# Kernel tuning notes

Hardware: AMD Instinct MI355X
Metric: run time of the kernel (lower is better)

Reference implementation:

```python
import jax, jax.numpy as jnp
import numpy as np

D_MODEL, D_K, D_V, N_HEADS = 1024, 64, 64, 16
BATCH, N_CTX = 2, 2048


def half_causal_allowed(n):
    # rows [0, n/2): attend to cols [0, n/2) only (dense block)
    # rows [n/2, n): standard causal (col <= row)
    i = jnp.arange(n)[:, None]
    j = jnp.arange(n)[None, :]
    top = (i < n // 2) & (j < n // 2)
    bot = (i >= n // 2) & (j <= i)
    return top | bot  # [n, n] bool


def setup_inputs() -> dict:
    key = jax.random.key(0)
    ks = jax.random.split(key, 8)
    s_in = 1.0 / np.sqrt(D_MODEL)
    s_out = 1.0 / np.sqrt(D_V * N_HEADS)
    return {
        "x": jax.random.normal(ks[0], (BATCH, N_CTX, D_MODEL), jnp.float32),
        # Linear weights stored [in, out] (transpose of torch layout)
        "Wq": jax.random.uniform(ks[1], (D_MODEL, D_K * N_HEADS), jnp.float32, -s_in, s_in),
        "bq": jax.random.uniform(ks[2], (D_K * N_HEADS,), jnp.float32, -s_in, s_in),
        "Wk": jax.random.uniform(ks[3], (D_MODEL, D_K * N_HEADS), jnp.float32, -s_in, s_in),
        "bk": jax.random.uniform(ks[4], (D_K * N_HEADS,), jnp.float32, -s_in, s_in),
        "Wv": jax.random.uniform(ks[5], (D_MODEL, D_V * N_HEADS), jnp.float32, -s_in, s_in),
        "bv": jax.random.uniform(ks[6], (D_V * N_HEADS,), jnp.float32, -s_in, s_in),
        "Wo": jax.random.uniform(ks[7], (D_V * N_HEADS, D_MODEL), jnp.float32, -s_out, s_out),
    }


def reference(x, Wq, bq, Wk, bk, Wv, bv, Wo):
    b, n, _ = x.shape
    h, dk, dv = N_HEADS, D_K, D_V
    # projections -> [b, h, n, d]
    q = (x @ Wq + bq).reshape(b, n, h, dk).transpose(0, 2, 1, 3)
    k = (x @ Wk + bk).reshape(b, n, h, dk).transpose(0, 2, 1, 3)
    v = (x @ Wv + bv).reshape(b, n, h, dv).transpose(0, 2, 1, 3)
    scores = jnp.einsum("bhqd,bhkd->bhqk", q / jnp.sqrt(jnp.float32(dk)), k)
    allowed = half_causal_allowed(n)  # [n, n]
    scores = jnp.where(allowed, scores, -jnp.inf)
    attn = jax.nn.softmax(scores, axis=-1)  # dropout p=0 -> identity
    out = jnp.einsum("bhqk,bhkd->bhqd", attn, v)
    out = out.transpose(0, 2, 1, 3).reshape(b, n, h * dv)
    return out @ Wo  # final Linear has no bias
```

## Files before the change

kernel.cpp:

```cpp
#include <hip/hip_runtime.h>
#include <hip/hip_bf16.h>

#define NH 16
#define DH 64
#define DM 1024
#define NC 2048
#define MROWS 4096
#define KVT 64

#define SCALE_Q 0.180336880f

typedef __attribute__((ext_vector_type(8))) short short8;
typedef __attribute__((ext_vector_type(4))) float f32x4;
typedef __attribute__((ext_vector_type(16))) float f32x16;
typedef __attribute__((ext_vector_type(4))) unsigned int uint4e;

__device__ __forceinline__ unsigned pkbf16(float a, float b) {
    unsigned r;
    asm("v_cvt_pk_bf16_f32 %0, %1, %2" : "=v"(r) : "v"(a), "v"(b));
    return r;
}
__device__ __forceinline__ unsigned short f2bf(float x) {
    return (unsigned short)(pkbf16(x, x) & 0xffffu);
}
__device__ __forceinline__ float exp2v(float x) {
    float r;
    asm("v_exp_f32 %0, %1" : "=v"(r) : "v"(x));
    return r;
}
__device__ __forceinline__ f32x16 fzero16() {
    f32x16 r;
    #pragma unroll
    for (int i = 0; i < 16; ++i) r[i] = 0.f;
    return r;
}
__device__ __forceinline__ short8 mk8(unsigned w0, unsigned w1, unsigned w2, unsigned w3) {
    uint4e u = {w0, w1, w2, w3};
    return __builtin_bit_cast(short8, u);
}
__device__ __forceinline__ void gload16(const unsigned short* g, unsigned short* l) {
    __builtin_amdgcn_global_load_lds(
        (const __attribute__((address_space(1))) void*)g,
        (__attribute__((address_space(3))) void*)l, 16, 0, 0);
}

__global__ __launch_bounds__(256) void cvt_x(const float* __restrict__ in,
                                             unsigned short* __restrict__ out, int n8)
{
    int i = blockIdx.x * 256 + threadIdx.x;
    if (i >= n8) return;
    const float4 a = ((const float4*)in)[i * 2];
    const float4 b = ((const float4*)in)[i * 2 + 1];
    uint4e u = {pkbf16(a.x, a.y), pkbf16(a.z, a.w), pkbf16(b.x, b.y), pkbf16(b.z, b.w)};
    ((uint4e*)out)[i] = u;
}

__global__ __launch_bounds__(256) void cvt_w4(const float* __restrict__ W0,
                                              const float* __restrict__ W1,
                                              const float* __restrict__ W2,
                                              const float* __restrict__ W3,
                                              unsigned short* __restrict__ Wt4)
{
    __shared__ unsigned short T[64][72];
    const int z = blockIdx.z;
    const float* W = (z == 0) ? W0 : (z == 1) ? W1 : (z == 2) ? W2 : W3;
    unsigned short* Wt = Wt4 + (size_t)z * DM * DM;
    const int t = threadIdx.x;
    const int r = t >> 2, s = t & 3;
    const int bi = blockIdx.y;
    const int bj = blockIdx.x;
    const float* src = W + (size_t)(bi * 64 + r) * DM + bj * 64 + s * 16;
    float4 f0 = ((const float4*)src)[0];
    float4 f1 = ((const float4*)src)[1];
    float4 f2 = ((const float4*)src)[2];
    float4 f3 = ((const float4*)src)[3];
    uint2 u;
    u.x = pkbf16(f0.x, f0.y); u.y = pkbf16(f0.z, f0.w); *(uint2*)&T[r][s * 16]      = u;
    u.x = pkbf16(f1.x, f1.y); u.y = pkbf16(f1.z, f1.w); *(uint2*)&T[r][s * 16 + 4]  = u;
    u.x = pkbf16(f2.x, f2.y); u.y = pkbf16(f2.z, f2.w); *(uint2*)&T[r][s * 16 + 8]  = u;
    u.x = pkbf16(f3.x, f3.y); u.y = pkbf16(f3.z, f3.w); *(uint2*)&T[r][s * 16 + 12] = u;
    __syncthreads();
    unsigned short vals[16];
    #pragma unroll
    for (int j = 0; j < 16; ++j) vals[j] = T[s * 16 + j][r];
    unsigned short* dst = Wt + (size_t)(bj * 64 + r) * DM + bi * 64 + s * 16;
    *(short8*)(dst)     = *(short8*)&vals[0];
    *(short8*)(dst + 8) = *(short8*)&vals[8];
}

__global__ __launch_bounds__(256) void gemm_qkv(const unsigned short* __restrict__ A,
                                                const unsigned short* __restrict__ Bt,
                                                const float* __restrict__ bq,
                                                const float* __restrict__ bk,
                                                const float* __restrict__ bv,
                                                unsigned short* __restrict__ Out)
{
    __shared__ unsigned short As[128 * 32];
    __shared__ unsigned short Bs[128 * 32];
    const int t  = threadIdx.x;
    const int w  = t >> 6, l = t & 63;
    const int wr = w >> 1, wc = w & 1;
    const int m0 = blockIdx.y << 7;
    const int n0 = blockIdx.x << 7;

    f32x4 acc[4][4] = {};
    const int nkt = DM >> 5;
    for (int kt = 0; kt < nkt; ++kt) {
        #pragma unroll
        for (int j = 0; j < 2; ++j) {
            const int c0 = j * 256 + w * 64;
            const int cc = c0 + l;
            const int row = cc >> 2, qq = cc & 3;
            gload16(A  + (size_t)(m0 + row) * DM + kt * 32 + qq * 8, &As[c0 * 8]);
            gload16(Bt + (size_t)(n0 + row) * DM + kt * 32 + qq * 8, &Bs[c0 * 8]);
        }
        __syncthreads();
        short8 af[4], bf_[4];
        #pragma unroll
        for (int mi = 0; mi < 4; ++mi)
            af[mi] = *(short8*)&As[(wr * 64 + mi * 16 + (l & 15)) * 32 + (l >> 4) * 8];
        #pragma unroll
        for (int ni = 0; ni < 4; ++ni)
            bf_[ni] = *(short8*)&Bs[(wc * 64 + ni * 16 + (l & 15)) * 32 + (l >> 4) * 8];
        #pragma unroll
        for (int mi = 0; mi < 4; ++mi)
            #pragma unroll
            for (int ni = 0; ni < 4; ++ni)
                acc[mi][ni] = __builtin_amdgcn_mfma_f32_16x16x32_bf16(
                                  af[mi], bf_[ni], acc[mi][ni], 0, 0, 0);
        __syncthreads();
    }

    const int seg = n0 >> 10;
    const float* bias = (seg == 0) ? bq : (seg == 1) ? bk : bv;
    const float scale = (seg == 0) ? SCALE_Q : 1.0f;
    const int ncol0 = (n0 & 1023) + wc * 64;
    float bvv[4];
    #pragma unroll
    for (int ni = 0; ni < 4; ++ni)
        bvv[ni] = bias[ncol0 + ni * 16 + (l & 15)];

    if (seg == 2) {
        unsigned short* vt = Out + 2 * (size_t)MROWS * DM;
        #pragma unroll
        for (int mi = 0; mi < 4; ++mi)
            #pragma unroll
            for (int ni = 0; ni < 4; ++ni) {
                const int gcol = ncol0 + ni * 16 + (l & 15);
                const int h_ = gcol >> 6, d_ = gcol & 63;
                #pragma unroll
                for (int r = 0; r < 4; ++r) {
                    const int grow = m0 + wr * 64 + mi * 16 + (l >> 4) * 4 + r;
                    const int b_ = grow >> 11, n_ = grow & 2047;
                    vt[(((size_t)b_ * 16 + h_) * 64 + d_) * NC + n_] =
                        f2bf(acc[mi][ni][r] + bvv[ni]);
                }
            }
    } else {
        unsigned short* C = Out + (size_t)seg * MROWS * DM;
        #pragma unroll
        for (int mi = 0; mi < 4; ++mi)
            #pragma unroll
            for (int ni = 0; ni < 4; ++ni) {
                const int gcol = ncol0 + ni * 16 + (l & 15);
                #pragma unroll
                for (int r = 0; r < 4; ++r) {
                    const int grow = m0 + wr * 64 + mi * 16 + (l >> 4) * 4 + r;
                    C[(size_t)grow * DM + gcol] = f2bf((acc[mi][ni][r] + bvv[ni]) * scale);
                }
            }
    }
}

__global__ __launch_bounds__(256) void gemm_wo(const unsigned short* __restrict__ A,
                                               const unsigned short* __restrict__ Bt,
                                               float* __restrict__ C)
{
    __shared__ unsigned short As[64 * 32];
    __shared__ unsigned short Bs[128 * 32];
    const int t = threadIdx.x, w = t >> 6, l = t & 63;
    const int wr = w >> 1, wc = w & 1;
    const int m0 = blockIdx.y << 6;
    const int n0 = blockIdx.x << 7;

    f32x4 acc[2][4] = {};
    const int nkt = DM >> 5;
    for (int kt = 0; kt < nkt; ++kt) {
        {
            const int c0 = w * 64;
            const int cc = c0 + l;
            const int row = cc >> 2, qq = cc & 3;
            gload16(A + (size_t)(m0 + row) * DM + kt * 32 + qq * 8, &As[c0 * 8]);
        }
        #pragma unroll
        for (int j = 0; j < 2; ++j) {
            const int c0 = j * 256 + w * 64;
            const int cc = c0 + l;
            const int row = cc >> 2, qq = cc & 3;
            gload16(Bt + (size_t)(n0 + row) * DM + kt * 32 + qq * 8, &Bs[c0 * 8]);
        }
        __syncthreads();
        short8 af[2], bf_[4];
        #pragma unroll
        for (int mi = 0; mi < 2; ++mi)
            af[mi] = *(short8*)&As[(wr * 32 + mi * 16 + (l & 15)) * 32 + (l >> 4) * 8];
        #pragma unroll
        for (int ni = 0; ni < 4; ++ni)
            bf_[ni] = *(short8*)&Bs[(wc * 64 + ni * 16 + (l & 15)) * 32 + (l >> 4) * 8];
        #pragma unroll
        for (int mi = 0; mi < 2; ++mi)
            #pragma unroll
            for (int ni = 0; ni < 4; ++ni)
                acc[mi][ni] = __builtin_amdgcn_mfma_f32_16x16x32_bf16(
                                  af[mi], bf_[ni], acc[mi][ni], 0, 0, 0);
        __syncthreads();
    }
    #pragma unroll
    for (int mi = 0; mi < 2; ++mi)
        #pragma unroll
        for (int ni = 0; ni < 4; ++ni) {
            const int gcol = n0 + wc * 64 + ni * 16 + (l & 15);
            #pragma unroll
            for (int r = 0; r < 4; ++r) {
                const int grow = m0 + wr * 32 + mi * 16 + (l >> 4) * 4 + r;
                C[(size_t)grow * DM + gcol] = acc[mi][ni][r];
            }
        }
}

__global__ __launch_bounds__(64, 2) void attn_sb(const unsigned short* __restrict__ Qg,
                                                 const unsigned short* __restrict__ Kg,
                                                 const unsigned short* __restrict__ Vtg,
                                                 unsigned short* __restrict__ Og)
{
    __shared__ unsigned short KS[4096];
    __shared__ unsigned short VS[4096];
    const int l   = threadIdx.x;
    const int l31 = l & 31;
    const int hi  = l >> 5;

    const int f   = blockIdx.x;
    const int xcd = f & 7;
    const int pos = f >> 3;
    const int bh  = xcd * 4 + (pos >> 6);
    int qt = pos & 63;
    if ((pos >> 6) & 1) qt = 63 - qt;
    const int b = bh >> 4;
    const int h = bh & 15;

    const int qb = qt << 5;
    const size_t rb0 = (size_t)b * NC;
    const int hd = h * DH;

    const unsigned short* qp = Qg + (rb0 + qb + l31) * DM + hd + hi * 8;
    short8 fq[4];
    #pragma unroll
    for (int c = 0; c < 4; ++c)
        fq[c] = *(const short8*)(qp + c * 16);

    f32x16 o0 = fzero16(), o1 = fzero16();
    float mrun = -1e30f, lrun = 0.f;
    const bool bottom = (qb >= NC / 2);
    const int nkv = bottom ? ((qt >> 1) + 1) : 16;

    const unsigned short* Vbase = Vtg + (size_t)bh * 64 * NC;

    auto stage = [&](int it) {
        const int kb = it * KVT;
        #pragma unroll
        for (int j = 0; j < 8; ++j) {
            const int p    = j * 64 + l;
            const int row  = p >> 3;
            const int slot = (p & 7) ^ (row & 7);
            gload16(Kg + (size_t)(rb0 + kb + row) * DM + hd + slot * 8,
                    &KS[j * 512]);
            gload16(Vbase + (size_t)row * NC + kb + slot * 8,
                    &VS[j * 512]);
        }
    };

    stage(0);

    for (int it = 0; it < nkv; ++it) {
        const int kb = it * KVT;
        asm volatile("s_waitcnt vmcnt(0)" ::: "memory");

        short8 kf[2][4], vf[2][4];
        #pragma unroll
        for (int half = 0; half < 2; ++half) {
            const int row = half * 32 + l31;
            const int rx  = row & 7;
            #pragma unroll
            for (int c = 0; c < 4; ++c) {
                const int slot = (c * 2 + hi) ^ rx;
                kf[half][c] = *(const short8*)(&KS[row * 64 + slot * 8]);
                vf[half][c] = *(const short8*)(&VS[row * 64 + slot * 8]);
            }
        }
        asm volatile("s_waitcnt lgkmcnt(0)" ::: "memory");
        __builtin_amdgcn_sched_barrier(0);
        if (it + 1 < nkv) stage(it + 1);

        f32x16 s0 = fzero16(), s1 = fzero16();
        __builtin_amdgcn_s_setprio(1);
        #pragma unroll
        for (int c = 0; c < 4; ++c) {
            s0 = __builtin_amdgcn_mfma_f32_32x32x16_bf16(kf[0][c], fq[c], s0, 0, 0, 0);
            s1 = __builtin_amdgcn_mfma_f32_32x32x16_bf16(kf[1][c], fq[c], s1, 0, 0, 0);
        }
        __builtin_amdgcn_s_setprio(0);

        if (bottom && it == nkv - 1) {
            const int qg = qb + l31;
            #pragma unroll
            for (int r = 0; r < 16; ++r) {
                const int kk = (r & 3) + 8 * (r >> 2) + 4 * hi;
                if (kb + kk > qg)      s0[r] = -1e30f;
                if (kb + 32 + kk > qg) s1[r] = -1e30f;
            }
        }
        float tm[16];
        #pragma unroll
        for (int r = 0; r < 16; ++r) tm[r] = fmaxf(s0[r], s1[r]);
        #pragma unroll
        for (int st = 8; st > 0; st >>= 1)
            #pragma unroll
            for (int r = 0; r < 8; ++r)
                if (r < st) tm[r] = fmaxf(tm[r], tm[r + st]);
        float pm = fmaxf(tm[0], __shfl_xor(tm[0], 32));
        if (!__all(pm - mrun <= 8.f)) {
            const float mnew = fmaxf(mrun, pm);
            const float corr = exp2v(mrun - mnew);
            mrun = mnew;
            lrun *= corr;
            #pragma unroll
            for (int i = 0; i < 16; ++i) { o0[i] *= corr; o1[i] *= corr; }
        }
        #pragma unroll
        for (int r = 0; r < 16; ++r) s0[r] = exp2v(s0[r] - mrun);
        #pragma unroll
        for (int r = 0; r < 16; ++r) s1[r] = exp2v(s1[r] - mrun);
        float t16[16];
        #pragma unroll
        for (int r = 0; r < 16; ++r) t16[r] = s0[r] + s1[r];
        #pragma unroll
        for (int st = 8; st > 0; st >>= 1)
            #pragma unroll
            for (int r = 0; r < 8; ++r)
                if (r < st) t16[r] += t16[r + st];
        lrun += t16[0] + __shfl_xor(t16[0], 32);

        __builtin_amdgcn_s_setprio(1);
        #pragma unroll
        for (int kc = 0; kc < 4; ++kc) {
            const f32x16 src = (kc < 2) ? s0 : s1;
            const int rbase = (kc & 1) * 8;
            unsigned A01 = pkbf16(src[rbase + 0], src[rbase + 1]);
            unsigned A23 = pkbf16(src[rbase + 2], src[rbase + 3]);
            unsigned A45 = pkbf16(src[rbase + 4], src[rbase + 5]);
            unsigned A67 = pkbf16(src[rbase + 6], src[rbase + 7]);
            unsigned s01 = (unsigned)__shfl_xor((int)A01, 32);
            unsigned s23 = (unsigned)__shfl_xor((int)A23, 32);
            unsigned s45 = (unsigned)__shfl_xor((int)A45, 32);
            unsigned s67 = (unsigned)__shfl_xor((int)A67, 32);
            short8 fp = hi ? mk8(s45, s67, A45, A67)
                           : mk8(A01, A23, s01, s23);
            o0 = __builtin_amdgcn_mfma_f32_32x32x16_bf16(vf[0][kc], fp, o0, 0, 0, 0);
            o1 = __builtin_amdgcn_mfma_f32_32x32x16_bf16(vf[1][kc], fp, o1, 0, 0, 0);
        }
        __builtin_amdgcn_s_setprio(0);
    }

    const float inv = 1.f / lrun;
    unsigned short* obuf = &KS[0];
    {
        unsigned short* reg = obuf + (size_t)l31 * 72;
        #pragma unroll
        for (int r = 0; r < 16; ++r) {
            const int dd = (r & 3) + 8 * (r >> 2) + 4 * hi;
            reg[dd]      = f2bf(o0[r] * inv);
            reg[dd + 32] = f2bf(o1[r] * inv);
        }
    }
    {
        const int row = l >> 1, seg = l & 1;
        const unsigned short* src = obuf + (size_t)row * 72 + seg * 32;
        unsigned short* dst = Og + (rb0 + qb + row) * DM + hd + seg * 32;
        #pragma unroll
        for (int i = 0; i < 4; ++i)
            *(short8*)(dst + i * 8) = *(const short8*)(src + i * 8);
    }
}

extern "C" void kernel_launch(void* const* d_in, const int* in_sizes, int n_in,
                              void* d_out, int out_size, void* d_ws, size_t ws_size,
                              hipStream_t stream)
{
    const float* x  = (const float*)d_in[0];
    const float* Wq = (const float*)d_in[1];
    const float* bq = (const float*)d_in[2];
    const float* Wk = (const float*)d_in[3];
    const float* bk = (const float*)d_in[4];
    const float* Wv = (const float*)d_in[5];
    const float* bv = (const float*)d_in[6];
    const float* Wo = (const float*)d_in[7];
    float* out = (float*)d_out;

    char* ws = (char*)d_ws;
    const size_t szA = (size_t)MROWS * DM * 2;
    const size_t szW = (size_t)DM * DM * 2;
    unsigned short* xb  = (unsigned short*)(ws);
    unsigned short* wqT = (unsigned short*)(ws + szA);
    unsigned short* woT = (unsigned short*)(ws + szA + 3 * szW);
    unsigned short* qb_ = (unsigned short*)(ws + szA + 4 * szW);
    unsigned short* kb_ = (unsigned short*)(ws + 2 * szA + 4 * szW);
    unsigned short* vt_ = (unsigned short*)(ws + 3 * szA + 4 * szW);
    unsigned short* ab_ = (unsigned short*)(ws + 4 * szA + 4 * szW);

    cvt_x<<<dim3(MROWS * DM / 8 / 256), 256, 0, stream>>>(x, xb, MROWS * DM / 8);
    cvt_w4<<<dim3(16, 16, 4), 256, 0, stream>>>(Wq, Wk, Wv, Wo, wqT);

    gemm_qkv<<<dim3(24, 32), 256, 0, stream>>>(xb, wqT, bq, bk, bv, qb_);
    attn_sb<<<dim3(2048), 64, 0, stream>>>(qb_, kb_, vt_, ab_);
    gemm_wo<<<dim3(8, 64), 256, 0, stream>>>(ab_, woT, out);
}
```

Baseline: 126.0 us.

## Store Q/K/V in MFMA fragment order and load attention operands directly from global

The QKV projection epilogue now writes Q, K and V into a pre-swizzled layout that matches the per-lane MFMA operand fragments. The attention kernel then reads K and V fragments straight from global memory into registers as contiguous 16-byte loads, with no LDS staging. K loads are double-buffered in registers across two iterations, and V is loaded at the start of each compute step. This removes LDS traffic and barriers from the attention loop. The costs are scattered 2-byte stores in the GEMM epilogue, a dropped occupancy hint, and global-load latency that is only partly hidden behind compute.

```diff
diff --git a/kernel.cpp b/kernel.cpp
--- a/kernel.cpp
+++ b/kernel.cpp
@@ -140,36 +140,34 @@
     for (int ni = 0; ni < 4; ++ni)
         bvv[ni] = bias[ncol0 + ni * 16 + (l & 15)];
 
-    if (seg == 2) {
-        unsigned short* vt = Out + 2 * (size_t)MROWS * DM;
-        #pragma unroll
-        for (int mi = 0; mi < 4; ++mi)
-            #pragma unroll
-            for (int ni = 0; ni < 4; ++ni) {
-                const int gcol = ncol0 + ni * 16 + (l & 15);
-                const int h_ = gcol >> 6, d_ = gcol & 63;
-                #pragma unroll
-                for (int r = 0; r < 4; ++r) {
-                    const int grow = m0 + wr * 64 + mi * 16 + (l >> 4) * 4 + r;
-                    const int b_ = grow >> 11, n_ = grow & 2047;
-                    vt[(((size_t)b_ * 16 + h_) * 64 + d_) * NC + n_] =
-                        f2bf(acc[mi][ni][r] + bvv[ni]);
+    unsigned short* dstQK = Out + (size_t)seg * MROWS * DM;
+    unsigned short* dstV  = Out + 2 * (size_t)MROWS * DM;
+
+    #pragma unroll
+    for (int mi = 0; mi < 4; ++mi)
+        #pragma unroll
+        for (int ni = 0; ni < 4; ++ni) {
+            const int gcol = ncol0 + ni * 16 + (l & 15);
+            const int h_ = gcol >> 6, d_ = gcol & 63;
+            #pragma unroll
+            for (int r = 0; r < 4; ++r) {
+                const int grow = m0 + wr * 64 + mi * 16 + (l >> 4) * 4 + r;
+                const int n  = grow & 2047;
+                const int bh = (grow >> 11) * 16 + h_;
+                const unsigned short val = f2bf((acc[mi][ni][r] + bvv[ni]) * scale);
+                if (seg <= 1) {
+                    const int g = n >> 5, rr = n & 31;
+                    const int c = d_ >> 4, h2 = (d_ >> 3) & 1, e = d_ & 7;
+                    dstQK[(((size_t)bh * 64 + g) * 4 + c) * 512 + (rr + 32 * h2) * 8 + e] = val;
+                } else {
+                    const int tt = n >> 6, nl = n & 63;
+                    const int kc = nl >> 4, h2 = (nl >> 3) & 1, e = nl & 7;
+                    const int half = d_ >> 5;
+                    dstV[((((size_t)bh * 32 + tt) * 2 + half) * 4 + kc) * 512 +
+                         ((d_ & 31) + 32 * h2) * 8 + e] = val;
                 }
             }
-    } else {
-        unsigned short* C = Out + (size_t)seg * MROWS * DM;
-        #pragma unroll
-        for (int mi = 0; mi < 4; ++mi)
-            #pragma unroll
-            for (int ni = 0; ni < 4; ++ni) {
-                const int gcol = ncol0 + ni * 16 + (l & 15);
-                #pragma unroll
-                for (int r = 0; r < 4; ++r) {
-                    const int grow = m0 + wr * 64 + mi * 16 + (l >> 4) * 4 + r;
-                    C[(size_t)grow * DM + gcol] = f2bf((acc[mi][ni][r] + bvv[ni]) * scale);
-                }
-            }
-    }
+        }
 }
 
 __global__ __launch_bounds__(256) void gemm_wo(const unsigned short* __restrict__ A,
@@ -228,13 +226,12 @@
         }
 }
 
-__global__ __launch_bounds__(64, 2) void attn_sb(const unsigned short* __restrict__ Qg,
-                                                 const unsigned short* __restrict__ Kg,
-                                                 const unsigned short* __restrict__ Vtg,
-                                                 unsigned short* __restrict__ Og)
-{
-    __shared__ unsigned short KS[4096];
-    __shared__ unsigned short VS[4096];
+__global__ __launch_bounds__(64) void attn_frag(const unsigned short* __restrict__ Qf,
+                                                const unsigned short* __restrict__ Kf,
+                                                const unsigned short* __restrict__ Vf,
+                                                unsigned short* __restrict__ Og)
+{
+    __shared__ unsigned short ob[32 * 72];
     const int l   = threadIdx.x;
     const int l31 = l & 31;
     const int hi  = l >> 5;
@@ -252,65 +249,47 @@
     const size_t rb0 = (size_t)b * NC;
     const int hd = h * DH;
 
-    const unsigned short* qp = Qg + (rb0 + qb + l31) * DM + hd + hi * 8;
+    const unsigned short* qfp = Qf + (((size_t)bh * 64 + qt) * 4) * 512 + l * 8;
     short8 fq[4];
     #pragma unroll
     for (int c = 0; c < 4; ++c)
-        fq[c] = *(const short8*)(qp + c * 16);
+        fq[c] = *(const short8*)(qfp + c * 512);
 
     f32x16 o0 = fzero16(), o1 = fzero16();
     float mrun = -1e30f, lrun = 0.f;
     const bool bottom = (qb >= NC / 2);
     const int nkv = bottom ? ((qt >> 1) + 1) : 16;
 
-    const unsigned short* Vbase = Vtg + (size_t)bh * 64 * NC;
-
-    auto stage = [&](int it) {
-        const int kb = it * KVT;
-        #pragma unroll
-        for (int j = 0; j < 8; ++j) {
-            const int p    = j * 64 + l;
-            const int row  = p >> 3;
-            const int slot = (p & 7) ^ (row & 7);
-            gload16(Kg + (size_t)(rb0 + kb + row) * DM + hd + slot * 8,
-                    &KS[j * 512]);
-            gload16(Vbase + (size_t)row * NC + kb + slot * 8,
-                    &VS[j * 512]);
-        }
+    const unsigned short* Kbase = Kf + ((size_t)bh * 64 * 4) * 512 + l * 8;
+    const unsigned short* Vbase = Vf + ((size_t)bh * 32 * 8) * 512 + l * 8;
+
+    auto loadK = [&](int it, short8* kf) {
+        #pragma unroll
+        for (int half = 0; half < 2; ++half)
+            #pragma unroll
+            for (int c = 0; c < 4; ++c)
+                kf[half * 4 + c] =
+                    *(const short8*)(Kbase + ((size_t)(it * 2 + half) * 4 + c) * 512);
     };
 
-    stage(0);
-
-    for (int it = 0; it < nkv; ++it) {
-        const int kb = it * KVT;
-        asm volatile("s_waitcnt vmcnt(0)" ::: "memory");
-
-        short8 kf[2][4], vf[2][4];
-        #pragma unroll
-        for (int half = 0; half < 2; ++half) {
-            const int row = half * 32 + l31;
-            const int rx  = row & 7;
-            #pragma unroll
-            for (int c = 0; c < 4; ++c) {
-                const int slot = (c * 2 + hi) ^ rx;
-                kf[half][c] = *(const short8*)(&KS[row * 64 + slot * 8]);
-                vf[half][c] = *(const short8*)(&VS[row * 64 + slot * 8]);
-            }
-        }
-        asm volatile("s_waitcnt lgkmcnt(0)" ::: "memory");
-        __builtin_amdgcn_sched_barrier(0);
-        if (it + 1 < nkv) stage(it + 1);
-
+    auto compute = [&](const short8* kf, int it, bool last) {
+        short8 vf[8];
+        #pragma unroll
+        for (int half = 0; half < 2; ++half)
+            #pragma unroll
+            for (int kc = 0; kc < 4; ++kc)
+                vf[half * 4 + kc] =
+                    *(const short8*)(Vbase + (((size_t)it * 2 + half) * 4 + kc) * 512);
         f32x16 s0 = fzero16(), s1 = fzero16();
         __builtin_amdgcn_s_setprio(1);
         #pragma unroll
         for (int c = 0; c < 4; ++c) {
-            s0 = __builtin_amdgcn_mfma_f32_32x32x16_bf16(kf[0][c], fq[c], s0, 0, 0, 0);
-            s1 = __builtin_amdgcn_mfma_f32_32x32x16_bf16(kf[1][c], fq[c], s1, 0, 0, 0);
+            s0 = __builtin_amdgcn_mfma_f32_32x32x16_bf16(kf[c],     fq[c], s0, 0, 0, 0);
+            s1 = __builtin_amdgcn_mfma_f32_32x32x16_bf16(kf[4 + c], fq[c], s1, 0, 0, 0);
         }
         __builtin_amdgcn_s_setprio(0);
-
-        if (bottom && it == nkv - 1) {
+        if (bottom && last) {
+            const int kb = it * KVT;
             const int qg = qb + l31;
             #pragma unroll
             for (int r = 0; r < 16; ++r) {
@@ -349,7 +328,6 @@
             for (int r = 0; r < 8; ++r)
                 if (r < st) t16[r] += t16[r + st];
         lrun += t16[0] + __shfl_xor(t16[0], 32);
-
         __builtin_amdgcn_s_setprio(1);
         #pragma unroll
         for (int kc = 0; kc < 4; ++kc) {
@@ -365,16 +343,27 @@
             unsigned s67 = (unsigned)__shfl_xor((int)A67, 32);
             short8 fp = hi ? mk8(s45, s67, A45, A67)
                            : mk8(A01, A23, s01, s23);
-            o0 = __builtin_amdgcn_mfma_f32_32x32x16_bf16(vf[0][kc], fp, o0, 0, 0, 0);
-            o1 = __builtin_amdgcn_mfma_f32_32x32x16_bf16(vf[1][kc], fp, o1, 0, 0, 0);
+            o0 = __builtin_amdgcn_mfma_f32_32x32x16_bf16(vf[kc],     fp, o0, 0, 0, 0);
+            o1 = __builtin_amdgcn_mfma_f32_32x32x16_bf16(vf[4 + kc], fp, o1, 0, 0, 0);
         }
         __builtin_amdgcn_s_setprio(0);
+    };
+
+    short8 ka[8], kb2[8];
+    loadK(0, ka);
+    for (int it = 0; it < nkv; it += 2) {
+        const bool hasB = (it + 1 < nkv);
+        if (hasB) loadK(it + 1, kb2);
+        compute(ka, it, it == nkv - 1);
+        if (hasB) {
+            if (it + 2 < nkv) loadK(it + 2, ka);
+            compute(kb2, it + 1, it + 1 == nkv - 1);
+        }
     }
 
     const float inv = 1.f / lrun;
-    unsigned short* obuf = &KS[0];
     {
-        unsigned short* reg = obuf + (size_t)l31 * 72;
+        unsigned short* reg = &ob[(size_t)l31 * 72];
         #pragma unroll
         for (int r = 0; r < 16; ++r) {
             const int dd = (r & 3) + 8 * (r >> 2) + 4 * hi;
@@ -384,7 +373,7 @@
     }
     {
         const int row = l >> 1, seg = l & 1;
-        const unsigned short* src = obuf + (size_t)row * 72 + seg * 32;
+        const unsigned short* src = &ob[(size_t)row * 72 + seg * 32];
         unsigned short* dst = Og + (rb0 + qb + row) * DM + hd + seg * 32;
         #pragma unroll
         for (int i = 0; i < 4; ++i)
@@ -412,15 +401,15 @@
     unsigned short* xb  = (unsigned short*)(ws);
     unsigned short* wqT = (unsigned short*)(ws + szA);
     unsigned short* woT = (unsigned short*)(ws + szA + 3 * szW);
-    unsigned short* qb_ = (unsigned short*)(ws + szA + 4 * szW);
-    unsigned short* kb_ = (unsigned short*)(ws + 2 * szA + 4 * szW);
-    unsigned short* vt_ = (unsigned short*)(ws + 3 * szA + 4 * szW);
+    unsigned short* qf_ = (unsigned short*)(ws + szA + 4 * szW);
+    unsigned short* kf_ = (unsigned short*)(ws + 2 * szA + 4 * szW);
+    unsigned short* vf_ = (unsigned short*)(ws + 3 * szA + 4 * szW);
     unsigned short* ab_ = (unsigned short*)(ws + 4 * szA + 4 * szW);
 
     cvt_x<<<dim3(MROWS * DM / 8 / 256), 256, 0, stream>>>(x, xb, MROWS * DM / 8);
     cvt_w4<<<dim3(16, 16, 4), 256, 0, stream>>>(Wq, Wk, Wv, Wo, wqT);
 
-    gemm_qkv<<<dim3(24, 32), 256, 0, stream>>>(xb, wqT, bq, bk, bv, qb_);
-    attn_sb<<<dim3(2048), 64, 0, stream>>>(qb_, kb_, vt_, ab_);
+    gemm_qkv<<<dim3(24, 32), 256, 0, stream>>>(xb, wqT, bq, bk, bv, qf_);
+    attn_frag<<<dim3(2048), 64, 0, stream>>>(qf_, kf_, vf_, ab_);
     gemm_wo<<<dim3(8, 64), 256, 0, stream>>>(ab_, woT, out);
 }
```

New measurement: 132.9 us. +5.4%, slower.
